# Kernel optimization log

Hardware: AMD Instinct MI355X
Metric: run time of the kernel (lower is better)

The kernel has to match this reference:

```python
import jax, jax.numpy as jnp
import numpy as np

B, T = 8, 16384
CLASSES, RC, EC = 256, 32, 256
NLAYERS = 40          # blocks(4) * layers(10)
DIL = 1024            # source uses 2**layers for every layer (faithful to code)
EPS = 1e-5


def _shift_right(x, d):
    # causal shift: y[t] = x[t-d], zero-padded
    return jnp.pad(x, ((0, 0), (0, 0), (d, 0)))[:, :, : x.shape[-1]]


def _conv1x1(x, w, b):
    # w: [out, in], x: [B, in, T]
    return jnp.einsum('oi,bit->bot', w, x) + b[None, :, None]


def _dconv2(x, w, b, d):
    # causal dilated conv, kernel 2: y[t] = w[:,:,0] x[t-d] + w[:,:,1] x[t] + b
    return (jnp.einsum('oi,bit->bot', w[:, :, 1], x)
            + jnp.einsum('oi,bit->bot', w[:, :, 0], _shift_right(x, d))
            + b[None, :, None])


def _bn(x, g, b):
    # training-mode BatchNorm1d: batch stats over (N, L)
    m = jnp.mean(x, axis=(0, 2), keepdims=True)
    v = jnp.var(x, axis=(0, 2), keepdims=True)
    return (x - m) * jax.lax.rsqrt(v + EPS) * g[None, :, None] + b[None, :, None]


def _mish(x):
    return x * jnp.tanh(jax.nn.softplus(x))


def setup_inputs() -> dict:
    key = jax.random.key(0)
    ks = jax.random.split(key, 16)
    n = jax.random.normal
    return {
        'x': n(ks[0], (B, CLASSES, T), jnp.float32),
        'start_w': n(ks[1], (RC, CLASSES), jnp.float32) * 0.05,
        'start_b': n(ks[2], (RC,), jnp.float32) * 0.05,
        'gt_w': n(ks[3], (NLAYERS, RC, RC, 2), jnp.float32) * 0.1,   # tanh branch
        'gt_b': n(ks[4], (NLAYERS, RC), jnp.float32) * 0.05,
        'gs_w': n(ks[5], (NLAYERS, RC, RC, 2), jnp.float32) * 0.1,   # sigmoid branch
        'gs_b': n(ks[6], (NLAYERS, RC), jnp.float32) * 0.05,
        'res_w': n(ks[7], (NLAYERS, RC, RC), jnp.float32) * 0.1,
        'res_b': n(ks[8], (NLAYERS, RC), jnp.float32) * 0.05,
        'bn_g': jnp.ones((NLAYERS, RC), jnp.float32),
        'bn_b': jnp.zeros((NLAYERS, RC), jnp.float32),
        'bn1_g': jnp.ones((RC,), jnp.float32),
        'bn1_b': jnp.zeros((RC,), jnp.float32),
        'e1_w': n(ks[9], (EC, RC), jnp.float32) * 0.1,
        'e1_b': n(ks[10], (EC,), jnp.float32) * 0.05,
        'bn2_g': jnp.ones((EC,), jnp.float32),
        'bn2_b': jnp.zeros((EC,), jnp.float32),
        'e2_w': n(ks[11], (CLASSES, EC), jnp.float32) * 0.05,
        'e2_b': n(ks[12], (CLASSES,), jnp.float32) * 0.05,
    }


def reference(x, start_w, start_b, gt_w, gt_b, gs_w, gs_b, res_w, res_b,
              bn_g, bn_b, bn1_g, bn1_b, e1_w, e1_b, bn2_g, bn2_b, e2_w, e2_b):
    # start_conv: CausalConv(classes, RC, k=1, shift=1) -> 1x1 conv on x shifted right by 1
    h = _conv1x1(_shift_right(x, 1), start_w, start_b)  # [B, RC, T]

    def step(carry, p):
        h, skip = carry
        gtw, gtb, gsw, gsb, rw, rb, bg, bb = p
        g = jnp.tanh(_dconv2(h, gtw, gtb, DIL)) * jax.nn.sigmoid(_dconv2(h, gsw, gsb, DIL))
        skip = skip + g
        h = h + _bn(_conv1x1(g, rw, rb), bg, bb)
        return (h, skip), None

    init = (h, jnp.zeros_like(h))
    (h, skip_sum), _ = jax.lax.scan(
        step, init, (gt_w, gt_b, gs_w, gs_b, res_w, res_b, bn_g, bn_b))

    y = _mish(_bn(skip_sum, bn1_g, bn1_b))
    y = _mish(_bn(_conv1x1(y, e1_w, e1_b), bn2_g, bn2_b))
    return _conv1x1(y, e2_w, e2_b)  # [B, CLASSES, T]
```

## Files before the change

### kernel.cpp

```cpp
#include <hip/hip_runtime.h>


#define EPSV 1e-5f
#define RN   (1.f/131072.f)

#define H_OFF  0
#define SK_OFF (4*1024*1024)
#define ST_OFF (8*1024*1024)
#define ST_SKIP 2560
#define ST_MU   2624
#define ST_Y    2656
#define ST_A2   3680
#define ST_B2   3936
#define ST_TOT  4192

__device__ __forceinline__ float rcp_f(float x) { return __builtin_amdgcn_rcpf(x); }
__device__ __forceinline__ float tanh_f(float x) {
    float e = __expf(2.f * x);
    return 1.f - 2.f * rcp_f(e + 1.f);
}
__device__ __forceinline__ float sigm_f(float x) { return rcp_f(1.f + __expf(-x)); }
__device__ __forceinline__ float mish_f(float x) {
    float e = __expf(x);
    float sp = (x > 15.f) ? x : __logf(1.f + e);
    return x * tanh_f(sp);
}

__global__ void k_zero(float* __restrict__ st) {
    int i = blockIdx.x * 256 + threadIdx.x;
    if (i < ST_TOT) st[i] = 0.f;
}

__global__ __launch_bounds__(256) void k_start(
        const float* __restrict__ x, const float* __restrict__ sw_g,
        const float* __restrict__ sb_g, float* __restrict__ h, float* __restrict__ skip)
{
    __shared__ float sw[256*36];
    __shared__ float sb[32];
    int tid = threadIdx.x, blk = blockIdx.x;
    int b = blk >> 6, r0 = (blk & 63) << 4;
    for (int k = tid; k < 8192; k += 256) {
        int o = k >> 8, c = k & 255;
        sw[c*36 + o] = sw_g[k];
    }
    if (tid < 32) sb[tid] = sb_g[tid];
    __syncthreads();

    int rr = tid & 15, s = tid >> 4;
    int t = r0 + rr + (s << 10);
    bool valid = (t >= 1);
    const float* xr = x + (long)b*256*16384 + (valid ? (t-1) : 0);
    float acc[32];
    #pragma unroll
    for (int o = 0; o < 32; ++o) acc[o] = 0.f;
    for (int c = 0; c < 256; ++c) {
        float xv = xr[(long)c*16384];
        xv = valid ? xv : 0.f;
        const float4* wrow = (const float4*)&sw[c*36];
        #pragma unroll
        for (int o4 = 0; o4 < 8; ++o4) {
            float4 w = wrow[o4];
            acc[o4*4+0] += w.x*xv; acc[o4*4+1] += w.y*xv;
            acc[o4*4+2] += w.z*xv; acc[o4*4+3] += w.w*xv;
        }
    }
    __syncthreads();
    #pragma unroll
    for (int o = 0; o < 32; ++o) sw[(rr*32 + o)*16 + s] = acc[o] + sb[o];
    __syncthreads();
    float4* hd = (float4*)(h + (long)blk*8192);
    float4* sd = (float4*)(skip + (long)blk*8192);
    const float4* ss = (const float4*)sw;
    float4 z4 = make_float4(0.f, 0.f, 0.f, 0.f);
    for (int k = tid; k < 2048; k += 256) { hd[k] = ss[k]; sd[k] = z4; }
}

__global__ __launch_bounds__(256) void k_layer(
        const float* __restrict__ gt_w, const float* __restrict__ gt_b,
        const float* __restrict__ gs_w, const float* __restrict__ gs_b,
        const float* __restrict__ res_w, const float* __restrict__ res_b,
        const float* __restrict__ bn_g, const float* __restrict__ bn_b,
        float* __restrict__ h, float* __restrict__ z, float* __restrict__ skip,
        float* __restrict__ st, int L)
{
    __shared__ float s_w[4096];
    __shared__ float s_r[1024];
    __shared__ float s_hg[4096];
    __shared__ float s_red[4][32][2];

    int tid = threadIdx.x;
    int o = tid & 31, chl = tid >> 5;
    long base = (long)blockIdx.x*4096 + chl*512 + o*16;

    for (int k = tid; k < 1024; k += 256) {
        int oo = k >> 5, ii = k & 31;
        float2 a = ((const float2*)(gt_w + (long)L*2048))[k];
        float2 c = ((const float2*)(gs_w + (long)L*2048))[k];
        float* d = &s_w[(ii*32 + oo)*4];
        d[0] = a.x; d[1] = a.y; d[2] = c.x; d[3] = c.y;
        s_r[ii*32 + oo] = res_w[(long)L*1024 + k];
    }

    float hreg[16];
    float4* hp4 = (float4*)(h + base);
    #pragma unroll
    for (int q = 0; q < 4; ++q) {
        float4 t4 = hp4[q];
        hreg[4*q+0]=t4.x; hreg[4*q+1]=t4.y; hreg[4*q+2]=t4.z; hreg[4*q+3]=t4.w;
    }
    if (L > 0) {
        float ssum = st[(L-1)*64 + o], ssq = st[(L-1)*64 + 32 + o];
        float m = ssum * RN;
        float v = ssq * RN - m*m;
        float a = rsqrtf(v + EPSV) * bn_g[(L-1)*32 + o];
        float bb = bn_b[(L-1)*32 + o] - m*a;
        const float4* zp4 = (const float4*)(z + base);
        #pragma unroll
        for (int q = 0; q < 4; ++q) {
            float4 t4 = zp4[q];
            hreg[4*q+0] += t4.x*a + bb; hreg[4*q+1] += t4.y*a + bb;
            hreg[4*q+2] += t4.z*a + bb; hreg[4*q+3] += t4.w*a + bb;
        }
        #pragma unroll
        for (int q = 0; q < 4; ++q)
            hp4[q] = make_float4(hreg[4*q], hreg[4*q+1], hreg[4*q+2], hreg[4*q+3]);
    }
    float4* hs4 = (float4*)&s_hg[chl*512 + o*16];
    #pragma unroll
    for (int q = 0; q < 4; ++q)
        hs4[q] = make_float4(hreg[4*q], hreg[4*q+1], hreg[4*q+2], hreg[4*q+3]);
    __syncthreads();

    float aT[16], aS[16];
    float gtb = gt_b[L*32 + o], gsb = gs_b[L*32 + o];
    #pragma unroll
    for (int s = 0; s < 16; ++s) { aT[s] = gtb; aS[s] = gsb; }
    #pragma unroll 4
    for (int i = 0; i < 32; ++i) {
        float4 w = *(const float4*)&s_w[(i*32 + o)*4];
        const float4* hr = (const float4*)&s_hg[chl*512 + i*16];
        float hp = 0.f;
        #pragma unroll
        for (int s4 = 0; s4 < 4; ++s4) {
            float4 hv = hr[s4];
            int s = 4*s4;
            aT[s+0] += w.y*hv.x + w.x*hp;   aS[s+0] += w.w*hv.x + w.z*hp;
            aT[s+1] += w.y*hv.y + w.x*hv.x; aS[s+1] += w.w*hv.y + w.z*hv.x;
            aT[s+2] += w.y*hv.z + w.x*hv.y; aS[s+2] += w.w*hv.z + w.z*hv.y;
            aT[s+3] += w.y*hv.w + w.x*hv.z; aS[s+3] += w.w*hv.w + w.z*hv.z;
            hp = hv.w;
        }
    }
    float g[16], sk[16];
    #pragma unroll
    for (int s = 0; s < 16; ++s) g[s] = tanh_f(aT[s]) * sigm_f(aS[s]);

    float4* skp4 = (float4*)(skip + base);
    #pragma unroll
    for (int q = 0; q < 4; ++q) {
        float4 t4 = skp4[q];
        sk[4*q+0] = t4.x + g[4*q+0]; sk[4*q+1] = t4.y + g[4*q+1];
        sk[4*q+2] = t4.z + g[4*q+2]; sk[4*q+3] = t4.w + g[4*q+3];
        skp4[q] = make_float4(sk[4*q], sk[4*q+1], sk[4*q+2], sk[4*q+3]);
    }

    __syncthreads();
    #pragma unroll
    for (int q = 0; q < 4; ++q)
        hs4[q] = make_float4(g[4*q], g[4*q+1], g[4*q+2], g[4*q+3]);
    __syncthreads();

    float az[16];
    float rbv = res_b[L*32 + o];
    #pragma unroll
    for (int s = 0; s < 16; ++s) az[s] = rbv;
    #pragma unroll 4
    for (int i = 0; i < 32; ++i) {
        float w = s_r[i*32 + o];
        const float4* gr = (const float4*)&s_hg[chl*512 + i*16];
        #pragma unroll
        for (int s4 = 0; s4 < 4; ++s4) {
            float4 gv = gr[s4];
            az[4*s4+0] += w*gv.x; az[4*s4+1] += w*gv.y;
            az[4*s4+2] += w*gv.z; az[4*s4+3] += w*gv.w;
        }
    }
    float4* zp4w = (float4*)(z + base);
    #pragma unroll
    for (int q = 0; q < 4; ++q)
        zp4w[q] = make_float4(az[4*q], az[4*q+1], az[4*q+2], az[4*q+3]);

    float ps = 0.f, pq = 0.f;
    #pragma unroll
    for (int s = 0; s < 16; ++s) { ps += az[s]; pq += az[s]*az[s]; }
    ps += __shfl_down(ps, 32); pq += __shfl_down(pq, 32);
    int wv = tid >> 6;
    if ((tid & 63) < 32) { s_red[wv][o][0] = ps; s_red[wv][o][1] = pq; }
    __syncthreads();
    if (tid < 32) {
        float a = s_red[0][tid][0] + s_red[1][tid][0] + s_red[2][tid][0] + s_red[3][tid][0];
        atomicAdd(&st[L*64 + tid], a);
    } else if (tid < 64) {
        int c = tid - 32;
        float a = s_red[0][c][1] + s_red[1][c][1] + s_red[2][c][1] + s_red[3][c][1];
        atomicAdd(&st[L*64 + 32 + c], a);
    }

    if (L == 39) {
        float p2 = 0.f, q2 = 0.f;
        #pragma unroll
        for (int s = 0; s < 16; ++s) { p2 += sk[s]; q2 += sk[s]*sk[s]; }
        p2 += __shfl_down(p2, 32); q2 += __shfl_down(q2, 32);
        __syncthreads();
        if ((tid & 63) < 32) { s_red[wv][o][0] = p2; s_red[wv][o][1] = q2; }
        __syncthreads();
        if (tid < 32) {
            float a = s_red[0][tid][0] + s_red[1][tid][0] + s_red[2][tid][0] + s_red[3][tid][0];
            atomicAdd(&st[ST_SKIP + tid], a);
        } else if (tid < 64) {
            int c = tid - 32;
            float a = s_red[0][c][1] + s_red[1][c][1] + s_red[2][c][1] + s_red[3][c][1];
            atomicAdd(&st[ST_SKIP + 32 + c], a);
        }
    }
}

__global__ __launch_bounds__(256) void k_ep_a(
        const float* __restrict__ skip, const float* __restrict__ bn1_g,
        const float* __restrict__ bn1_b, float* __restrict__ st)
{
    __shared__ float sy[256*33];
    __shared__ float sA[32], sB[32];
    int tid = threadIdx.x;
    long cb = (long)blockIdx.x * 8192;
    if (tid < 32) {
        float ssum = st[ST_SKIP + tid], ssq = st[ST_SKIP + 32 + tid];
        float m = ssum * RN, v = ssq * RN - m*m;
        float a = rsqrtf(v + EPSV) * bn1_g[tid];
        sA[tid] = a; sB[tid] = bn1_b[tid] - m*a;
    }
    __syncthreads();
    for (int k = tid; k < 8192; k += 256) {
        int i = k & 31, p = k >> 5;
        int rr = p & 15, s = p >> 4;
        float v = skip[cb + rr*512 + i*16 + s];
        sy[p*33 + i] = mish_f(v * sA[i] + sB[i]);
    }
    __syncthreads();
    if (tid < 32) {
        float mu = 0.f;
        for (int p = 0; p < 256; ++p) mu += sy[p*33 + tid];
        atomicAdd(&st[ST_MU + tid], mu);
    }
    int jj = tid & 31, i0 = tid >> 5;
    float a0 = 0.f, a1 = 0.f, a2 = 0.f, a3 = 0.f;
    for (int p = 0; p < 256; ++p) {
        float yj = sy[p*33 + jj];
        a0 += yj * sy[p*33 + i0];
        a1 += yj * sy[p*33 + i0 + 8];
        a2 += yj * sy[p*33 + i0 + 16];
        a3 += yj * sy[p*33 + i0 + 24];
    }
    atomicAdd(&st[ST_Y + (i0     )*32 + jj], a0);
    atomicAdd(&st[ST_Y + (i0 +  8)*32 + jj], a1);
    atomicAdd(&st[ST_Y + (i0 + 16)*32 + jj], a2);
    atomicAdd(&st[ST_Y + (i0 + 24)*32 + jj], a3);
}

__global__ void k_ep_b(
        const float* __restrict__ e1_w, const float* __restrict__ e1_b,
        const float* __restrict__ bn2_g, const float* __restrict__ bn2_b,
        float* __restrict__ st)
{
    __shared__ float mu[32];
    int o = threadIdx.x;
    if (o < 32) mu[o] = st[ST_MU + o] * RN;
    __syncthreads();
    float w[32];
    const float4* wr = (const float4*)(e1_w + o*32);
    #pragma unroll
    for (int q = 0; q < 8; ++q) {
        float4 t4 = wr[q];
        w[4*q]=t4.x; w[4*q+1]=t4.y; w[4*q+2]=t4.z; w[4*q+3]=t4.w;
    }
    float m2 = e1_b[o];
    #pragma unroll
    for (int i = 0; i < 32; ++i) m2 += w[i]*mu[i];
    float var = 0.f;
    for (int i = 0; i < 32; ++i) {
        float wi = w[i], mi = mu[i];
        for (int j = 0; j < 32; ++j)
            var += wi * w[j] * (st[ST_Y + i*32 + j]*RN - mi*mu[j]);
    }
    float a2 = rsqrtf(var + EPSV) * bn2_g[o];
    st[ST_A2 + o] = a2;
    st[ST_B2 + o] = bn2_b[o] - m2*a2;
}

__global__ __launch_bounds__(256, 4) void k_ep_c(
        const float* __restrict__ skip,
        const float* __restrict__ bn1_g, const float* __restrict__ bn1_b,
        const float* __restrict__ e1_w, const float* __restrict__ e1_b,
        const float* __restrict__ e2_w, const float* __restrict__ e2_b,
        const float* __restrict__ st, float* __restrict__ out)
{
    __shared__ float y1l[32*32];
    __shared__ float y2l[256*36];
    __shared__ float sA[32], sB[32];
    int tid = threadIdx.x;
    int blk = blockIdx.x;
    int b = blk >> 6, r0 = (blk & 63) << 4;
    long cb = (long)blk * 8192;
    if (tid < 32) {
        float ssum = st[ST_SKIP + tid], ssq = st[ST_SKIP + 32 + tid];
        float m = ssum * RN, v = ssq * RN - m*m;
        float a = rsqrtf(v + EPSV) * bn1_g[tid];
        sA[tid] = a; sB[tid] = bn1_b[tid] - m*a;
    }
    float w1[32];
    {
        const float4* wr = (const float4*)(e1_w + tid*32);
        #pragma unroll
        for (int q = 0; q < 8; ++q) {
            float4 t4 = wr[q];
            w1[4*q]=t4.x; w1[4*q+1]=t4.y; w1[4*q+2]=t4.z; w1[4*q+3]=t4.w;
        }
    }
    float a2 = st[ST_A2 + tid], b2 = st[ST_B2 + tid];
    float eb1 = e1_b[tid];
    float eb2 = e2_b[tid];
    const float4* w2row = (const float4*)(e2_w + (long)tid * 256);
    __syncthreads();

    for (int st8 = 0; st8 < 8; ++st8) {
        for (int k = tid; k < 1024; k += 256) {
            int i = k >> 5, q = k & 31;
            int rr = q & 15, sl = q >> 4;
            float v = skip[cb + rr*512 + i*16 + st8*2 + sl];
            y1l[i*32 + q] = mish_f(v * sA[i] + sB[i]);
        }
        __syncthreads();
        #pragma unroll 2
        for (int q4 = 0; q4 < 8; ++q4) {
            float4 acc = make_float4(eb1, eb1, eb1, eb1);
            #pragma unroll 8
            for (int i = 0; i < 32; ++i) {
                float4 yv = *(const float4*)&y1l[i*32 + q4*4];
                float wi = w1[i];
                acc.x += wi*yv.x; acc.y += wi*yv.y; acc.z += wi*yv.z; acc.w += wi*yv.w;
            }
            float4 y2v;
            y2v.x = mish_f(acc.x*a2 + b2);
            y2v.y = mish_f(acc.y*a2 + b2);
            y2v.z = mish_f(acc.z*a2 + b2);
            y2v.w = mish_f(acc.w*a2 + b2);
            *(float4*)&y2l[tid*36 + q4*4] = y2v;
        }
        __syncthreads();
        float acc[32];
        #pragma unroll
        for (int q = 0; q < 32; ++q) acc[q] = eb2;
        for (int i4 = 0; i4 < 64; ++i4) {
            float4 w4 = w2row[i4];
            float wa[4] = {w4.x, w4.y, w4.z, w4.w};
            #pragma unroll
            for (int ii = 0; ii < 4; ++ii) {
                float wv = wa[ii];
                const float* yr = &y2l[(i4*4 + ii)*36];
                #pragma unroll
                for (int q4 = 0; q4 < 8; ++q4) {
                    float4 yv = *(const float4*)&yr[q4*4];
                    acc[q4*4+0] += wv*yv.x; acc[q4*4+1] += wv*yv.y;
                    acc[q4*4+2] += wv*yv.z; acc[q4*4+3] += wv*yv.w;
                }
            }
        }
        long ob = ((long)b*256 + tid)*16384 + (long)(st8*2)*1024 + r0;
        float4* op = (float4*)&out[ob];
        op[0] = make_float4(acc[0],  acc[1],  acc[2],  acc[3]);
        op[1] = make_float4(acc[4],  acc[5],  acc[6],  acc[7]);
        op[2] = make_float4(acc[8],  acc[9],  acc[10], acc[11]);
        op[3] = make_float4(acc[12], acc[13], acc[14], acc[15]);
        float4* op2 = (float4*)&out[ob + 1024];
        op2[0] = make_float4(acc[16], acc[17], acc[18], acc[19]);
        op2[1] = make_float4(acc[20], acc[21], acc[22], acc[23]);
        op2[2] = make_float4(acc[24], acc[25], acc[26], acc[27]);
        op2[3] = make_float4(acc[28], acc[29], acc[30], acc[31]);
    }
}

extern "C" void kernel_launch(void* const* d_in, const int* in_sizes, int n_in,
                              void* d_out, int out_size, void* d_ws, size_t ws_size,
                              hipStream_t stream) {
    const float* x       = (const float*)d_in[0];
    const float* start_w = (const float*)d_in[1];
    const float* start_b = (const float*)d_in[2];
    const float* gt_w    = (const float*)d_in[3];
    const float* gt_b    = (const float*)d_in[4];
    const float* gs_w    = (const float*)d_in[5];
    const float* gs_b    = (const float*)d_in[6];
    const float* res_w   = (const float*)d_in[7];
    const float* res_b   = (const float*)d_in[8];
    const float* bn_g    = (const float*)d_in[9];
    const float* bn_b    = (const float*)d_in[10];
    const float* bn1_g   = (const float*)d_in[11];
    const float* bn1_b   = (const float*)d_in[12];
    const float* e1_w    = (const float*)d_in[13];
    const float* e1_b    = (const float*)d_in[14];
    const float* bn2_g   = (const float*)d_in[15];
    const float* bn2_b   = (const float*)d_in[16];
    const float* e2_w    = (const float*)d_in[17];
    const float* e2_b    = (const float*)d_in[18];
    float* ws  = (float*)d_ws;
    float* out = (float*)d_out;

    float* h    = ws + H_OFF;
    float* skip = ws + SK_OFF;
    float* st   = ws + ST_OFF;
    size_t need_full = ((size_t)ST_OFF + 8192 + 4*1024*1024) * 4;
    float* z = (ws_size >= need_full) ? (ws + ST_OFF + 8192)
                                      : (float*)d_out;

    k_zero<<<dim3(17), dim3(256), 0, stream>>>(st);
    k_start<<<dim3(512), dim3(256), 0, stream>>>(x, start_w, start_b, h, skip);
    for (int L = 0; L < 40; ++L)
        k_layer<<<dim3(1024), dim3(256), 0, stream>>>(
            gt_w, gt_b, gs_w, gs_b, res_w, res_b, bn_g, bn_b, h, z, skip, st, L);
    k_ep_a<<<dim3(512), dim3(256), 0, stream>>>(skip, bn1_g, bn1_b, st);
    k_ep_b<<<dim3(1), dim3(256), 0, stream>>>(e1_w, e1_b, bn2_g, bn2_b, st);
    k_ep_c<<<dim3(512), dim3(256), 0, stream>>>(skip, bn1_g, bn1_b, e1_w, e1_b,
                                                e2_w, e2_b, st, out);
}
```

Baseline: 2.687 ms.

## Fuse all 40 WaveNet layers into one persistent cooperative kernel with grid barriers

Replaces 40 per-layer launches with a single persistent kernel of 512 blocks. Each block keeps its h tile (8192 floats) and skip accumulators on chip across all layers, and synchronises BatchNorm statistics through a two-level atomic-counter grid barrier. This removes the per-layer global round trips for h, z and skip plus the launch overhead, at the cost of 40 grid-wide barriers and a dependency on all blocks being co-resident. The epilogue kernel is also split into 4096 blocks instead of looping eight slices per block, and the scratch counters are placed in the output buffer.

```diff
diff --git a/kernel.cpp b/kernel.cpp
--- a/kernel.cpp
+++ b/kernel.cpp
@@ -14,6 +14,14 @@
 #define ST_B2   3936
 #define ST_TOT  4192
 
+#define SZ_STAT (40*4096)
+#define CTR0    SZ_STAT
+#define ROOT0   (CTR0 + 40*16*32)
+#define DONE0   (ROOT0 + 40*32)
+#define SCR_TOT (DONE0 + 40*32)
+
+#define NBLK 512
+
 __device__ __forceinline__ float rcp_f(float x) { return __builtin_amdgcn_rcpf(x); }
 __device__ __forceinline__ float tanh_f(float x) {
     float e = __expf(2.f * x);
@@ -26,14 +34,15 @@
     return x * tanh_f(sp);
 }
 
-__global__ void k_zero(float* __restrict__ st) {
+__global__ void k_zero(float* __restrict__ st, float* __restrict__ scr) {
     int i = blockIdx.x * 256 + threadIdx.x;
-    if (i < ST_TOT) st[i] = 0.f;
+    if (i < SCR_TOT) scr[i] = 0.f;
+    if (i < ST_TOT)  st[i]  = 0.f;
 }
 
 __global__ __launch_bounds__(256) void k_start(
         const float* __restrict__ x, const float* __restrict__ sw_g,
-        const float* __restrict__ sb_g, float* __restrict__ h, float* __restrict__ skip)
+        const float* __restrict__ sb_g, float* __restrict__ h)
 {
     __shared__ float sw[256*36];
     __shared__ float sb[32];
@@ -69,159 +78,184 @@
     for (int o = 0; o < 32; ++o) sw[(rr*32 + o)*16 + s] = acc[o] + sb[o];
     __syncthreads();
     float4* hd = (float4*)(h + (long)blk*8192);
-    float4* sd = (float4*)(skip + (long)blk*8192);
     const float4* ss = (const float4*)sw;
-    float4 z4 = make_float4(0.f, 0.f, 0.f, 0.f);
-    for (int k = tid; k < 2048; k += 256) { hd[k] = ss[k]; sd[k] = z4; }
-}
-
-__global__ __launch_bounds__(256) void k_layer(
+    for (int k = tid; k < 2048; k += 256) hd[k] = ss[k];
+}
+
+__global__ __launch_bounds__(256, 3) void k_layers(
         const float* __restrict__ gt_w, const float* __restrict__ gt_b,
         const float* __restrict__ gs_w, const float* __restrict__ gs_b,
         const float* __restrict__ res_w, const float* __restrict__ res_b,
         const float* __restrict__ bn_g, const float* __restrict__ bn_b,
-        float* __restrict__ h, float* __restrict__ z, float* __restrict__ skip,
-        float* __restrict__ st, int L)
+        const float* __restrict__ h, float* __restrict__ skip,
+        float* __restrict__ scr, float* __restrict__ st)
 {
-    __shared__ float s_w[4096];
+    __shared__ float s_h[8192];
+    __shared__ float s_wg[4096];
     __shared__ float s_r[1024];
-    __shared__ float s_hg[4096];
     __shared__ float s_red[4][32][2];
+    unsigned* ctr = (unsigned*)scr;
 
     int tid = threadIdx.x;
-    int o = tid & 31, chl = tid >> 5;
-    long base = (long)blockIdx.x*4096 + chl*512 + o*16;
-
-    for (int k = tid; k < 1024; k += 256) {
-        int oo = k >> 5, ii = k & 31;
-        float2 a = ((const float2*)(gt_w + (long)L*2048))[k];
-        float2 c = ((const float2*)(gs_w + (long)L*2048))[k];
-        float* d = &s_w[(ii*32 + oo)*4];
-        d[0] = a.x; d[1] = a.y; d[2] = c.x; d[3] = c.y;
-        s_r[ii*32 + oo] = res_w[(long)L*1024 + k];
-    }
-
-    float hreg[16];
-    float4* hp4 = (float4*)(h + base);
-    #pragma unroll
-    for (int q = 0; q < 4; ++q) {
-        float4 t4 = hp4[q];
-        hreg[4*q+0]=t4.x; hreg[4*q+1]=t4.y; hreg[4*q+2]=t4.z; hreg[4*q+3]=t4.w;
-    }
-    if (L > 0) {
-        float ssum = st[(L-1)*64 + o], ssq = st[(L-1)*64 + 32 + o];
+    int o = tid & 31, chl = tid >> 5, wv = tid >> 6;
+    long base = (long)blockIdx.x*8192 + chl*512 + o*16;
+
+    #pragma unroll
+    for (int t = 0; t < 2; ++t) {
+        const float4* hp4 = (const float4*)(h + base + t*4096);
+        float4* hs4 = (float4*)&s_h[t*4096 + chl*512 + o*16];
+        #pragma unroll
+        for (int q = 0; q < 4; ++q) hs4[q] = hp4[q];
+    }
+    float sk[2][16];
+    #pragma unroll
+    for (int t = 0; t < 2; ++t)
+        #pragma unroll
+        for (int s = 0; s < 16; ++s) sk[t][s] = 0.f;
+
+    for (int L = 0; L < 40; ++L) {
+        for (int k = tid; k < 1024; k += 256) {
+            int oo = k >> 5, ii = k & 31;
+            float2 a = ((const float2*)(gt_w + (long)L*2048))[k];
+            float2 c = ((const float2*)(gs_w + (long)L*2048))[k];
+            float* d = &s_wg[(ii*32 + oo)*4];
+            d[0] = a.x; d[1] = a.y; d[2] = c.x; d[3] = c.y;
+            s_r[ii*32 + oo] = res_w[(long)L*1024 + k];
+        }
+        __syncthreads();
+
+        float g0[16], g1[16];
+        float gtb = gt_b[L*32 + o], gsb = gs_b[L*32 + o];
+        #pragma unroll
+        for (int t = 0; t < 2; ++t) {
+            float aT[16], aS[16];
+            #pragma unroll
+            for (int s = 0; s < 16; ++s) { aT[s] = gtb; aS[s] = gsb; }
+            #pragma unroll 4
+            for (int i = 0; i < 32; ++i) {
+                float4 w = *(const float4*)&s_wg[(i*32 + o)*4];
+                const float4* hr = (const float4*)&s_h[t*4096 + chl*512 + i*16];
+                float hp = 0.f;
+                #pragma unroll
+                for (int s4 = 0; s4 < 4; ++s4) {
+                    float4 hv = hr[s4];
+                    int s = 4*s4;
+                    aT[s+0] += w.y*hv.x + w.x*hp;   aS[s+0] += w.w*hv.x + w.z*hp;
+                    aT[s+1] += w.y*hv.y + w.x*hv.x; aS[s+1] += w.w*hv.y + w.z*hv.x;
+                    aT[s+2] += w.y*hv.z + w.x*hv.y; aS[s+2] += w.w*hv.z + w.z*hv.y;
+                    aT[s+3] += w.y*hv.w + w.x*hv.z; aS[s+3] += w.w*hv.w + w.z*hv.z;
+                    hp = hv.w;
+                }
+            }
+            float* gd = t ? g1 : g0;
+            #pragma unroll
+            for (int s = 0; s < 16; ++s) {
+                gd[s] = tanh_f(aT[s]) * sigm_f(aS[s]);
+                sk[t][s] += gd[s];
+            }
+        }
+        __syncthreads();
+
+        float az[2][16];
+        float rbv = res_b[L*32 + o];
+        float ps = 0.f, pq = 0.f;
+        #pragma unroll
+        for (int t = 0; t < 2; ++t) {
+            const float* gsrc = t ? g1 : g0;
+            float4* gw = (float4*)&s_wg[chl*512 + o*16];
+            #pragma unroll
+            for (int q = 0; q < 4; ++q)
+                gw[q] = make_float4(gsrc[4*q], gsrc[4*q+1], gsrc[4*q+2], gsrc[4*q+3]);
+            __syncthreads();
+            #pragma unroll
+            for (int s = 0; s < 16; ++s) az[t][s] = rbv;
+            #pragma unroll 4
+            for (int i = 0; i < 32; ++i) {
+                float w = s_r[i*32 + o];
+                const float4* gr = (const float4*)&s_wg[chl*512 + i*16];
+                #pragma unroll
+                for (int s4 = 0; s4 < 4; ++s4) {
+                    float4 gv = gr[s4];
+                    az[t][4*s4+0] += w*gv.x; az[t][4*s4+1] += w*gv.y;
+                    az[t][4*s4+2] += w*gv.z; az[t][4*s4+3] += w*gv.w;
+                }
+            }
+            #pragma unroll
+            for (int s = 0; s < 16; ++s) { ps += az[t][s]; pq += az[t][s]*az[t][s]; }
+            __syncthreads();
+        }
+
+        ps += __shfl_down(ps, 32); pq += __shfl_down(pq, 32);
+        if ((tid & 63) < 32) { s_red[wv][o][0] = ps; s_red[wv][o][1] = pq; }
+        __syncthreads();
+        if (tid < 32) {
+            float a_ = s_red[0][tid][0] + s_red[1][tid][0] + s_red[2][tid][0] + s_red[3][tid][0];
+            atomicAdd(&scr[(long)L*4096 + tid*64], a_);
+            __threadfence();
+        } else if (tid < 64) {
+            int c = tid - 32;
+            float a_ = s_red[0][c][1] + s_red[1][c][1] + s_red[2][c][1] + s_red[3][c][1];
+            atomicAdd(&scr[(long)L*4096 + c*64 + 32], a_);
+            __threadfence();
+        }
+        __syncthreads();
+
+        if (tid == 0) {
+            int leaf = blockIdx.x & 15;
+            unsigned old = __hip_atomic_fetch_add(&ctr[CTR0 + (L*16 + leaf)*32], 1u,
+                                                  __ATOMIC_ACQ_REL, __HIP_MEMORY_SCOPE_AGENT);
+            if (old == (NBLK/16 - 1)) {
+                unsigned r = __hip_atomic_fetch_add(&ctr[ROOT0 + L*32], 1u,
+                                                    __ATOMIC_ACQ_REL, __HIP_MEMORY_SCOPE_AGENT);
+                if (r == 15)
+                    __hip_atomic_store(&ctr[DONE0 + L*32], 1u,
+                                       __ATOMIC_RELEASE, __HIP_MEMORY_SCOPE_AGENT);
+            }
+            while (__hip_atomic_load(&ctr[DONE0 + L*32],
+                                     __ATOMIC_ACQUIRE, __HIP_MEMORY_SCOPE_AGENT) == 0u)
+                __builtin_amdgcn_s_sleep(8);
+        }
+        __syncthreads();
+
+        float ssum = __hip_atomic_load(&scr[(long)L*4096 + o*64],
+                                       __ATOMIC_RELAXED, __HIP_MEMORY_SCOPE_AGENT);
+        float ssq  = __hip_atomic_load(&scr[(long)L*4096 + o*64 + 32],
+                                       __ATOMIC_RELAXED, __HIP_MEMORY_SCOPE_AGENT);
         float m = ssum * RN;
         float v = ssq * RN - m*m;
-        float a = rsqrtf(v + EPSV) * bn_g[(L-1)*32 + o];
-        float bb = bn_b[(L-1)*32 + o] - m*a;
-        const float4* zp4 = (const float4*)(z + base);
-        #pragma unroll
-        for (int q = 0; q < 4; ++q) {
-            float4 t4 = zp4[q];
-            hreg[4*q+0] += t4.x*a + bb; hreg[4*q+1] += t4.y*a + bb;
-            hreg[4*q+2] += t4.z*a + bb; hreg[4*q+3] += t4.w*a + bb;
-        }
-        #pragma unroll
-        for (int q = 0; q < 4; ++q)
-            hp4[q] = make_float4(hreg[4*q], hreg[4*q+1], hreg[4*q+2], hreg[4*q+3]);
-    }
-    float4* hs4 = (float4*)&s_hg[chl*512 + o*16];
-    #pragma unroll
-    for (int q = 0; q < 4; ++q)
-        hs4[q] = make_float4(hreg[4*q], hreg[4*q+1], hreg[4*q+2], hreg[4*q+3]);
-    __syncthreads();
-
-    float aT[16], aS[16];
-    float gtb = gt_b[L*32 + o], gsb = gs_b[L*32 + o];
-    #pragma unroll
-    for (int s = 0; s < 16; ++s) { aT[s] = gtb; aS[s] = gsb; }
-    #pragma unroll 4
-    for (int i = 0; i < 32; ++i) {
-        float4 w = *(const float4*)&s_w[(i*32 + o)*4];
-        const float4* hr = (const float4*)&s_hg[chl*512 + i*16];
-        float hp = 0.f;
-        #pragma unroll
-        for (int s4 = 0; s4 < 4; ++s4) {
-            float4 hv = hr[s4];
-            int s = 4*s4;
-            aT[s+0] += w.y*hv.x + w.x*hp;   aS[s+0] += w.w*hv.x + w.z*hp;
-            aT[s+1] += w.y*hv.y + w.x*hv.x; aS[s+1] += w.w*hv.y + w.z*hv.x;
-            aT[s+2] += w.y*hv.z + w.x*hv.y; aS[s+2] += w.w*hv.z + w.z*hv.y;
-            aT[s+3] += w.y*hv.w + w.x*hv.z; aS[s+3] += w.w*hv.w + w.z*hv.z;
-            hp = hv.w;
-        }
-    }
-    float g[16], sk[16];
-    #pragma unroll
-    for (int s = 0; s < 16; ++s) g[s] = tanh_f(aT[s]) * sigm_f(aS[s]);
-
-    float4* skp4 = (float4*)(skip + base);
-    #pragma unroll
-    for (int q = 0; q < 4; ++q) {
-        float4 t4 = skp4[q];
-        sk[4*q+0] = t4.x + g[4*q+0]; sk[4*q+1] = t4.y + g[4*q+1];
-        sk[4*q+2] = t4.z + g[4*q+2]; sk[4*q+3] = t4.w + g[4*q+3];
-        skp4[q] = make_float4(sk[4*q], sk[4*q+1], sk[4*q+2], sk[4*q+3]);
-    }
-
-    __syncthreads();
-    #pragma unroll
-    for (int q = 0; q < 4; ++q)
-        hs4[q] = make_float4(g[4*q], g[4*q+1], g[4*q+2], g[4*q+3]);
-    __syncthreads();
-
-    float az[16];
-    float rbv = res_b[L*32 + o];
-    #pragma unroll
-    for (int s = 0; s < 16; ++s) az[s] = rbv;
-    #pragma unroll 4
-    for (int i = 0; i < 32; ++i) {
-        float w = s_r[i*32 + o];
-        const float4* gr = (const float4*)&s_hg[chl*512 + i*16];
-        #pragma unroll
-        for (int s4 = 0; s4 < 4; ++s4) {
-            float4 gv = gr[s4];
-            az[4*s4+0] += w*gv.x; az[4*s4+1] += w*gv.y;
-            az[4*s4+2] += w*gv.z; az[4*s4+3] += w*gv.w;
-        }
-    }
-    float4* zp4w = (float4*)(z + base);
-    #pragma unroll
-    for (int q = 0; q < 4; ++q)
-        zp4w[q] = make_float4(az[4*q], az[4*q+1], az[4*q+2], az[4*q+3]);
-
-    float ps = 0.f, pq = 0.f;
-    #pragma unroll
-    for (int s = 0; s < 16; ++s) { ps += az[s]; pq += az[s]*az[s]; }
-    ps += __shfl_down(ps, 32); pq += __shfl_down(pq, 32);
-    int wv = tid >> 6;
-    if ((tid & 63) < 32) { s_red[wv][o][0] = ps; s_red[wv][o][1] = pq; }
+        float a = rsqrtf(v + EPSV) * bn_g[L*32 + o];
+        float bb = bn_b[L*32 + o] - m*a;
+        #pragma unroll
+        for (int t = 0; t < 2; ++t) {
+            float* hrow = &s_h[t*4096 + chl*512 + o*16];
+            #pragma unroll
+            for (int s = 0; s < 16; ++s) hrow[s] += az[t][s]*a + bb;
+        }
+    }
+
+    float p2 = 0.f, q2 = 0.f;
+    #pragma unroll
+    for (int t = 0; t < 2; ++t)
+        #pragma unroll
+        for (int s = 0; s < 16; ++s) { p2 += sk[t][s]; q2 += sk[t][s]*sk[t][s]; }
+    p2 += __shfl_down(p2, 32); q2 += __shfl_down(q2, 32);
+    __syncthreads();
+    if ((tid & 63) < 32) { s_red[wv][o][0] = p2; s_red[wv][o][1] = q2; }
     __syncthreads();
     if (tid < 32) {
-        float a = s_red[0][tid][0] + s_red[1][tid][0] + s_red[2][tid][0] + s_red[3][tid][0];
-        atomicAdd(&st[L*64 + tid], a);
+        float a_ = s_red[0][tid][0] + s_red[1][tid][0] + s_red[2][tid][0] + s_red[3][tid][0];
+        atomicAdd(&st[ST_SKIP + tid], a_);
     } else if (tid < 64) {
         int c = tid - 32;
-        float a = s_red[0][c][1] + s_red[1][c][1] + s_red[2][c][1] + s_red[3][c][1];
-        atomicAdd(&st[L*64 + 32 + c], a);
-    }
-
-    if (L == 39) {
-        float p2 = 0.f, q2 = 0.f;
-        #pragma unroll
-        for (int s = 0; s < 16; ++s) { p2 += sk[s]; q2 += sk[s]*sk[s]; }
-        p2 += __shfl_down(p2, 32); q2 += __shfl_down(q2, 32);
-        __syncthreads();
-        if ((tid & 63) < 32) { s_red[wv][o][0] = p2; s_red[wv][o][1] = q2; }
-        __syncthreads();
-        if (tid < 32) {
-            float a = s_red[0][tid][0] + s_red[1][tid][0] + s_red[2][tid][0] + s_red[3][tid][0];
-            atomicAdd(&st[ST_SKIP + tid], a);
-        } else if (tid < 64) {
-            int c = tid - 32;
-            float a = s_red[0][c][1] + s_red[1][c][1] + s_red[2][c][1] + s_red[3][c][1];
-            atomicAdd(&st[ST_SKIP + 32 + c], a);
-        }
+        float a_ = s_red[0][c][1] + s_red[1][c][1] + s_red[2][c][1] + s_red[3][c][1];
+        atomicAdd(&st[ST_SKIP + 32 + c], a_);
+    }
+    #pragma unroll
+    for (int t = 0; t < 2; ++t) {
+        float4* skp = (float4*)(skip + base + t*4096);
+        #pragma unroll
+        for (int q = 0; q < 4; ++q)
+            skp[q] = make_float4(sk[t][4*q], sk[t][4*q+1], sk[t][4*q+2], sk[t][4*q+3]);
     }
 }
 
@@ -308,7 +342,7 @@
     __shared__ float y2l[256*36];
     __shared__ float sA[32], sB[32];
     int tid = threadIdx.x;
-    int blk = blockIdx.x;
+    int blk = blockIdx.x >> 3, st8 = blockIdx.x & 7;
     int b = blk >> 6, r0 = (blk & 63) << 4;
     long cb = (long)blk * 8192;
     if (tid < 32) {
@@ -332,61 +366,59 @@
     const float4* w2row = (const float4*)(e2_w + (long)tid * 256);
     __syncthreads();
 
-    for (int st8 = 0; st8 < 8; ++st8) {
-        for (int k = tid; k < 1024; k += 256) {
-            int i = k >> 5, q = k & 31;
-            int rr = q & 15, sl = q >> 4;
-            float v = skip[cb + rr*512 + i*16 + st8*2 + sl];
-            y1l[i*32 + q] = mish_f(v * sA[i] + sB[i]);
-        }
-        __syncthreads();
-        #pragma unroll 2
-        for (int q4 = 0; q4 < 8; ++q4) {
-            float4 acc = make_float4(eb1, eb1, eb1, eb1);
-            #pragma unroll 8
-            for (int i = 0; i < 32; ++i) {
-                float4 yv = *(const float4*)&y1l[i*32 + q4*4];
-                float wi = w1[i];
-                acc.x += wi*yv.x; acc.y += wi*yv.y; acc.z += wi*yv.z; acc.w += wi*yv.w;
+    for (int k = tid; k < 1024; k += 256) {
+        int i = k >> 5, q = k & 31;
+        int rr = q & 15, sl = q >> 4;
+        float v = skip[cb + rr*512 + i*16 + st8*2 + sl];
+        y1l[i*32 + q] = mish_f(v * sA[i] + sB[i]);
+    }
+    __syncthreads();
+    #pragma unroll 2
+    for (int q4 = 0; q4 < 8; ++q4) {
+        float4 acc = make_float4(eb1, eb1, eb1, eb1);
+        #pragma unroll 8
+        for (int i = 0; i < 32; ++i) {
+            float4 yv = *(const float4*)&y1l[i*32 + q4*4];
+            float wi = w1[i];
+            acc.x += wi*yv.x; acc.y += wi*yv.y; acc.z += wi*yv.z; acc.w += wi*yv.w;
+        }
+        float4 y2v;
+        y2v.x = mish_f(acc.x*a2 + b2);
+        y2v.y = mish_f(acc.y*a2 + b2);
+        y2v.z = mish_f(acc.z*a2 + b2);
+        y2v.w = mish_f(acc.w*a2 + b2);
+        *(float4*)&y2l[tid*36 + q4*4] = y2v;
+    }
+    __syncthreads();
+    float acc[32];
+    #pragma unroll
+    for (int q = 0; q < 32; ++q) acc[q] = eb2;
+    for (int i4 = 0; i4 < 64; ++i4) {
+        float4 w4 = w2row[i4];
+        float wa[4] = {w4.x, w4.y, w4.z, w4.w};
+        #pragma unroll
+        for (int ii = 0; ii < 4; ++ii) {
+            float wv = wa[ii];
+            const float* yr = &y2l[(i4*4 + ii)*36];
+            #pragma unroll
+            for (int q4 = 0; q4 < 8; ++q4) {
+                float4 yv = *(const float4*)&yr[q4*4];
+                acc[q4*4+0] += wv*yv.x; acc[q4*4+1] += wv*yv.y;
+                acc[q4*4+2] += wv*yv.z; acc[q4*4+3] += wv*yv.w;
             }
-            float4 y2v;
-            y2v.x = mish_f(acc.x*a2 + b2);
-            y2v.y = mish_f(acc.y*a2 + b2);
-            y2v.z = mish_f(acc.z*a2 + b2);
-            y2v.w = mish_f(acc.w*a2 + b2);
-            *(float4*)&y2l[tid*36 + q4*4] = y2v;
-        }
-        __syncthreads();
-        float acc[32];
-        #pragma unroll
-        for (int q = 0; q < 32; ++q) acc[q] = eb2;
-        for (int i4 = 0; i4 < 64; ++i4) {
-            float4 w4 = w2row[i4];
-            float wa[4] = {w4.x, w4.y, w4.z, w4.w};
-            #pragma unroll
-            for (int ii = 0; ii < 4; ++ii) {
-                float wv = wa[ii];
-                const float* yr = &y2l[(i4*4 + ii)*36];
-                #pragma unroll
-                for (int q4 = 0; q4 < 8; ++q4) {
-                    float4 yv = *(const float4*)&yr[q4*4];
-                    acc[q4*4+0] += wv*yv.x; acc[q4*4+1] += wv*yv.y;
-                    acc[q4*4+2] += wv*yv.z; acc[q4*4+3] += wv*yv.w;
-                }
-            }
-        }
-        long ob = ((long)b*256 + tid)*16384 + (long)(st8*2)*1024 + r0;
-        float4* op = (float4*)&out[ob];
-        op[0] = make_float4(acc[0],  acc[1],  acc[2],  acc[3]);
-        op[1] = make_float4(acc[4],  acc[5],  acc[6],  acc[7]);
-        op[2] = make_float4(acc[8],  acc[9],  acc[10], acc[11]);
-        op[3] = make_float4(acc[12], acc[13], acc[14], acc[15]);
-        float4* op2 = (float4*)&out[ob + 1024];
-        op2[0] = make_float4(acc[16], acc[17], acc[18], acc[19]);
-        op2[1] = make_float4(acc[20], acc[21], acc[22], acc[23]);
-        op2[2] = make_float4(acc[24], acc[25], acc[26], acc[27]);
-        op2[3] = make_float4(acc[28], acc[29], acc[30], acc[31]);
-    }
+        }
+    }
+    long ob = ((long)b*256 + tid)*16384 + (long)(st8*2)*1024 + r0;
+    float4* op = (float4*)&out[ob];
+    op[0] = make_float4(acc[0],  acc[1],  acc[2],  acc[3]);
+    op[1] = make_float4(acc[4],  acc[5],  acc[6],  acc[7]);
+    op[2] = make_float4(acc[8],  acc[9],  acc[10], acc[11]);
+    op[3] = make_float4(acc[12], acc[13], acc[14], acc[15]);
+    float4* op2 = (float4*)&out[ob + 1024];
+    op2[0] = make_float4(acc[16], acc[17], acc[18], acc[19]);
+    op2[1] = make_float4(acc[20], acc[21], acc[22], acc[23]);
+    op2[2] = make_float4(acc[24], acc[25], acc[26], acc[27]);
+    op2[3] = make_float4(acc[28], acc[29], acc[30], acc[31]);
 }
 
 extern "C" void kernel_launch(void* const* d_in, const int* in_sizes, int n_in,
@@ -417,17 +449,29 @@
     float* h    = ws + H_OFF;
     float* skip = ws + SK_OFF;
     float* st   = ws + ST_OFF;
-    size_t need_full = ((size_t)ST_OFF + 8192 + 4*1024*1024) * 4;
-    float* z = (ws_size >= need_full) ? (ws + ST_OFF + 8192)
-                                      : (float*)d_out;
-
-    k_zero<<<dim3(17), dim3(256), 0, stream>>>(st);
-    k_start<<<dim3(512), dim3(256), 0, stream>>>(x, start_w, start_b, h, skip);
-    for (int L = 0; L < 40; ++L)
-        k_layer<<<dim3(1024), dim3(256), 0, stream>>>(
-            gt_w, gt_b, gs_w, gs_b, res_w, res_b, bn_g, bn_b, h, z, skip, st, L);
+    float* scr  = out;
+
+    k_zero<<<dim3(730), dim3(256), 0, stream>>>(st, scr);
+    k_start<<<dim3(512), dim3(256), 0, stream>>>(x, start_w, start_b, h);
+
+    {
+        const float* hc = h;
+        void* kargs[12] = {
+            (void*)&gt_w, (void*)&gt_b, (void*)&gs_w, (void*)&gs_b,
+            (void*)&res_w, (void*)&res_b, (void*)&bn_g, (void*)&bn_b,
+            (void*)&hc, (void*)&skip, (void*)&scr, (void*)&st };
+        hipError_t rc = hipLaunchCooperativeKernel((const void*)k_layers,
+                                                   dim3(NBLK), dim3(256),
+                                                   kargs, 0, stream);
+        if (rc != hipSuccess) {
+            k_layers<<<dim3(NBLK), dim3(256), 0, stream>>>(
+                gt_w, gt_b, gs_w, gs_b, res_w, res_b, bn_g, bn_b,
+                h, skip, scr, st);
+        }
+    }
+
     k_ep_a<<<dim3(512), dim3(256), 0, stream>>>(skip, bn1_g, bn1_b, st);
     k_ep_b<<<dim3(1), dim3(256), 0, stream>>>(e1_w, e1_b, bn2_g, bn2_b, st);
-    k_ep_c<<<dim3(512), dim3(256), 0, stream>>>(skip, bn1_g, bn1_b, e1_w, e1_b,
-                                                e2_w, e2_b, st, out);
-}
+    k_ep_c<<<dim3(4096), dim3(256), 0, stream>>>(skip, bn1_g, bn1_b, e1_w, e1_b,
+                                                 e2_w, e2_b, st, out);
+}
```

Measured after the change: 3.582 ms. 33.3% more time.
